# Optimization experiments

Hardware: AMD Instinct MI355X
Metric: run time of the kernel (lower is better)

The kernel has to match this reference:

```python
import jax, jax.numpy as jnp
import numpy as np
import math

B, SES, SEQ, H, K = 16, 16, 64, 512, 32
L = SES * SEQ


def setup_inputs() -> dict:
    key = jax.random.key(0)
    ks = jax.random.split(key, 16)
    s = 1.0 / math.sqrt(H)
    return {
        "user_emb": jax.random.normal(ks[0], (B, H), jnp.float32),
        "item_emb": jax.random.normal(ks[1], (B, SES, SEQ, H), jnp.float32),
        "mask": jnp.zeros((B, L, K), jnp.float32),
        "index": jax.random.randint(ks[2], (L, K), 0, L, jnp.int64),
        "Wq": jax.random.normal(ks[3], (H, H), jnp.float32) * s,
        "bq": jnp.zeros((H,), jnp.float32),
        "Wk": jax.random.normal(ks[4], (H, H), jnp.float32) * s,
        "bk": jnp.zeros((H,), jnp.float32),
        "Wv": jax.random.normal(ks[5], (H, H), jnp.float32) * s,
        "bv": jnp.zeros((H,), jnp.float32),
        "Wd": jax.random.normal(ks[6], (H, H), jnp.float32) * s,
        "bd": jnp.zeros((H,), jnp.float32),
        "ln_g": jnp.ones((H,), jnp.float32),
        "ln_b": jnp.zeros((H,), jnp.float32),
    }


def reference(user_emb, item_emb, mask, index, Wq, bq, Wk, bk, Wv, bv, Wd, bd, ln_g, ln_b):
    b, ses, seq, h = item_emb.shape
    l = ses * seq
    item_flat = item_emb.reshape(b, l, h)
    q = user_emb @ Wq.T + bq                       # [B, H]
    k = item_flat @ Wk.T + bk                      # [B, L, H]
    v = item_flat @ Wv.T + bv                      # [B, L, H]
    # scalar query against all L keys, scaled by sqrt(hidden_size)
    scores = jnp.einsum("bh,blh->bl", q, k) / math.sqrt(h)
    scores = scores[:, index] + mask               # gather -> [B, L, K]
    w = jax.nn.softmax(scores, axis=-1)            # [B, L, K]
    vg = v[:, index, :]                            # gather -> [B, L, K, H]
    attn_out = jnp.einsum("blk,blkh->blh", w, vg)  # [B, L, H]
    dense = attn_out @ Wd.T + bd
    x = dense + item_flat                          # residual (dropout = identity, eval)
    mu = jnp.mean(x, axis=-1, keepdims=True)
    var = jnp.var(x, axis=-1, keepdims=True)
    y = (x - mu) / jnp.sqrt(var + 1e-12) * ln_g + ln_b
    return y.reshape(b, ses, seq, h)
```

## Files before the change

### kernel.cpp

```cpp
#include <hip/hip_runtime.h>
#include <math.h>

constexpr int HD   = 512;
constexpr int LL   = 1024;
constexpr int MT   = 16384;
constexpr int KNBR = 32;
constexpr float SCL = 0.04419417382415922f;

typedef __attribute__((ext_vector_type(8))) short  bf16x8;
typedef __attribute__((ext_vector_type(4))) float  f32x4;

__device__ inline float b2f(unsigned short u) {
    union { unsigned int i; float f; } v; v.i = (unsigned int)u << 16; return v.f;
}
__device__ inline float b2f_lo(unsigned int u) {
    union { unsigned int i; float f; } v; v.i = u << 16; return v.f;
}
__device__ inline float b2f_hi(unsigned int u) {
    union { unsigned int i; float f; } v; v.i = u & 0xffff0000u; return v.f;
}
__device__ inline unsigned short f2b(float x) {
    union { float f; unsigned int u; } v; v.f = x;
    unsigned int r = v.u + 0x7fff + ((v.u >> 16) & 1);
    return (unsigned short)(r >> 16);
}

constexpr int PB_CONV_I = 8192;
constexpr int PB_CONV_W = 512;
constexpr int PB_Q      = 2048;

__global__ __launch_bounds__(256) void prep(
    const float* __restrict__ item, const float* __restrict__ Wv,
    const float* __restrict__ Wd, const float* __restrict__ u,
    const float* __restrict__ Wq, const float* __restrict__ bq,
    unsigned short* __restrict__ item_bf, unsigned short* __restrict__ item_kt,
    unsigned short* __restrict__ Wv_bf, unsigned short* __restrict__ Wd_bf,
    float* __restrict__ q)
{
    const int blk = blockIdx.x, tid = threadIdx.x;

    if (blk < PB_CONV_I) {
        const int i = blk * 1024 + tid * 4;
        float4 v = *(const float4*)&item[i];
        ushort4 o;
        o.x = f2b(v.x); o.y = f2b(v.y); o.z = f2b(v.z); o.w = f2b(v.w);
        *(ushort4*)&item_bf[i] = o;
        const int m = i >> 9, k = i & 511;
        *(ushort4*)&item_kt[((size_t)(k >> 5) * MT + m) * 32 + (k & 31)] = o;
        return;
    }
    if (blk < PB_CONV_I + PB_CONV_W) {
        const int n = HD*HD;
        const int i = (blk - PB_CONV_I) * 1024 + tid * 4;
        const float* s; unsigned short* d; int off;
        if (i < n) { s = Wv; d = Wv_bf; off = i; }
        else       { s = Wd; d = Wd_bf; off = i - n; }
        float4 v = *(const float4*)&s[off];
        ushort4 o;
        o.x = f2b(v.x); o.y = f2b(v.y); o.z = f2b(v.z); o.w = f2b(v.w);
        const int nr = off >> 9, k = off & 511;
        *(ushort4*)&d[((k >> 5) * 512 + nr) * 32 + (k & 31)] = o;
        return;
    }
    {
        const int wid  = (blk - PB_CONV_I - PB_CONV_W) * 4 + (tid >> 6);
        const int lane = tid & 63;
        const int b = wid >> 9, h = wid & 511;
        const float* ur = &u[b*HD + lane*8];
        const float* wr = &Wq[(size_t)h*HD + lane*8];
        const float4 u0 = *(const float4*)ur, u1 = *(const float4*)(ur+4);
        const float4 w0 = *(const float4*)wr, w1 = *(const float4*)(wr+4);
        float acc = u0.x*w0.x + u0.y*w0.y + u0.z*w0.z + u0.w*w0.w
                  + u1.x*w1.x + u1.y*w1.y + u1.z*w1.z + u1.w*w1.w;
        #pragma unroll
        for (int off = 32; off; off >>= 1) acc += __shfl_down(acc, off);
        if (lane == 0) q[b*HD + h] = acc + bq[h];
    }
}

__global__ __launch_bounds__(256) void gemm_v_r(
    const unsigned short* __restrict__ Akt, const unsigned short* __restrict__ Wt,
    const float* __restrict__ bv, const float* __restrict__ Wk,
    const float* __restrict__ bk, const float* __restrict__ q,
    unsigned short* __restrict__ v_bf, float* __restrict__ rbuf,
    float* __restrict__ s0buf)
{
    __shared__ unsigned short As[2][128 * 32];
    __shared__ unsigned short Bs[2][128 * 32];

    const int blk = blockIdx.x;
    const int tid = threadIdx.x;

    if (blk >= 512) {
        if (blk < 640) {
            __shared__ float red[4][64];
            const int rblk = blk - 512;
            const int b = rblk >> 3, c0 = (rblk & 7) * 64;
            const int cl = tid & 63, hg = tid >> 6;
            const float* qb = &q[b*HD];
            const float* wb = &Wk[(size_t)hg*128*HD + c0 + cl];
            float acc = 0.f;
            #pragma unroll 8
            for (int h = 0; h < 128; h++)
                acc += qb[hg*128 + h] * wb[(size_t)h*HD];
            red[hg][cl] = acc;
            __syncthreads();
            if (tid < 64)
                rbuf[b*HD + c0 + tid] = SCL *
                    (red[0][tid] + red[1][tid] + red[2][tid] + red[3][tid]);
        } else {
            __shared__ float sp[4];
            const int b = blk - 640;
            float p = q[b*HD + tid]*bk[tid] + q[b*HD + tid + 256]*bk[tid + 256];
            #pragma unroll
            for (int off = 32; off; off >>= 1) p += __shfl_down(p, off);
            if ((tid & 63) == 0) sp[tid >> 6] = p;
            __syncthreads();
            if (tid == 0) s0buf[b] = (sp[0] + sp[1] + sp[2] + sp[3]) * SCL;
        }
        return;
    }

    const int rowb = (blk & 7) | ((blk >> 5) << 3);
    const int colb = (blk >> 3) & 3;
    const int row0 = rowb * 128;
    const int col0 = colb * 128;

    const int wave = tid >> 6, lane = tid & 63;
    const int wm = (wave >> 1) * 64;
    const int wn = (wave & 1)  * 64;

    const int lrr = lane >> 2;
    const int cc  = lane & 3;
    int st_row[2], st_gchunk[2];
    #pragma unroll
    for (int t = 0; t < 2; t++) {
        const int m = wave*32 + t*16 + lrr;
        st_row[t]    = m;
        st_gchunk[t] = cc ^ ((m >> 1) & 3);
    }

    const int fr   = lane & 15;
    const int quad = lane >> 4;

    f32x4 acc[4][4];
    #pragma unroll
    for (int i = 0; i < 4; i++)
        #pragma unroll
        for (int j = 0; j < 4; j++)
            acc[i][j] = (f32x4){0.f, 0.f, 0.f, 0.f};

    int a_off[4], b_off[4];
    #pragma unroll
    for (int i = 0; i < 4; i++) {
        const int m = wm + i*16 + fr;
        a_off[i] = m*32 + ((quad ^ ((m >> 1) & 3)) << 3);
        const int n = wn + i*16 + fr;
        b_off[i] = n*32 + ((quad ^ ((n >> 1) & 3)) << 3);
    }

    auto stage = [&](int bf, int kt) {
        #pragma unroll
        for (int t = 0; t < 2; t++) {
            const int m = st_row[t];
            const unsigned short* ga =
                &Akt[((size_t)kt*MT + row0 + m)*32 + st_gchunk[t]*8];
            __builtin_amdgcn_global_load_lds(
                (const __attribute__((address_space(1))) void*)ga,
                (__attribute__((address_space(3))) void*)&As[bf][(wave*32 + t*16)*32],
                16, 0, 0);
            const unsigned short* gw =
                &Wt[((size_t)kt*512 + col0 + m)*32 + st_gchunk[t]*8];
            __builtin_amdgcn_global_load_lds(
                (const __attribute__((address_space(1))) void*)gw,
                (__attribute__((address_space(3))) void*)&Bs[bf][(wave*32 + t*16)*32],
                16, 0, 0);
        }
    };

    stage(0, 0);
    stage(1, 1);

    for (int s = 0; s < 15; ++s) {
        asm volatile("s_waitcnt vmcnt(4)" ::: "memory");
        __builtin_amdgcn_s_barrier();
        asm volatile("" ::: "memory");

        const int cur = s & 1;
        bf16x8 af[4], bfr[4];
        #pragma unroll
        for (int i = 0; i < 4; i++) {
            af[i]  = *(const bf16x8*)&As[cur][a_off[i]];
            bfr[i] = *(const bf16x8*)&Bs[cur][b_off[i]];
        }
        asm volatile("s_waitcnt lgkmcnt(0)" ::: "memory");
        __builtin_amdgcn_sched_barrier(0);
        __builtin_amdgcn_s_barrier();

        if (s + 2 < 16) stage(cur, s + 2);

        __builtin_amdgcn_s_setprio(1);
        #pragma unroll
        for (int i = 0; i < 4; i++)
            #pragma unroll
            for (int j = 0; j < 4; j++)
                acc[i][j] = __builtin_amdgcn_mfma_f32_16x16x32_bf16(
                    af[i], bfr[j], acc[i][j], 0, 0, 0);
        __builtin_amdgcn_s_setprio(0);
    }
    {
        asm volatile("s_waitcnt vmcnt(0)" ::: "memory");
        __builtin_amdgcn_s_barrier();
        asm volatile("" ::: "memory");
        bf16x8 af[4], bfr[4];
        #pragma unroll
        for (int i = 0; i < 4; i++) {
            af[i]  = *(const bf16x8*)&As[1][a_off[i]];
            bfr[i] = *(const bf16x8*)&Bs[1][b_off[i]];
        }
        asm volatile("s_waitcnt lgkmcnt(0)" ::: "memory");
        __builtin_amdgcn_sched_barrier(0);
        #pragma unroll
        for (int i = 0; i < 4; i++)
            #pragma unroll
            for (int j = 0; j < 4; j++)
                acc[i][j] = __builtin_amdgcn_mfma_f32_16x16x32_bf16(
                    af[i], bfr[j], acc[i][j], 0, 0, 0);
    }

    #pragma unroll
    for (int j = 0; j < 4; j++) {
        const int col = col0 + wn + j*16 + fr;
        const float bb = bv[col];
        #pragma unroll
        for (int i = 0; i < 4; i++) {
            #pragma unroll
            for (int r = 0; r < 4; r++) {
                const int row = row0 + wm + i*16 + quad*4 + r;
                v_bf[(size_t)row*HD + col] = f2b(acc[i][j][r] + bb);
            }
        }
    }
}

__global__ __launch_bounds__(256) void gp_scores(
    const float* __restrict__ rbuf, const float* __restrict__ s0buf,
    const unsigned short* __restrict__ item_bf, float* __restrict__ scores)
{
    const int m = blockIdx.x * 4 + (threadIdx.x >> 6);
    const int lane = threadIdx.x & 63;
    const int b = m >> 10;
    const unsigned short* ir = &item_bf[(size_t)m*HD + lane*8];
    const uint4 iv = *(const uint4*)ir;
    const float* rr = &rbuf[b*HD + lane*8];
    const float4 r0 = *(const float4*)rr;
    const float4 r1 = *(const float4*)(rr + 4);
    float acc = r0.x*b2f_lo(iv.x) + r0.y*b2f_hi(iv.x)
              + r0.z*b2f_lo(iv.y) + r0.w*b2f_hi(iv.y)
              + r1.x*b2f_lo(iv.z) + r1.y*b2f_hi(iv.z)
              + r1.z*b2f_lo(iv.w) + r1.w*b2f_hi(iv.w);
    #pragma unroll
    for (int off = 32; off; off >>= 1) acc += __shfl_down(acc, off);
    if (lane == 0) scores[m] = acc + s0buf[b];
}

__global__ __launch_bounds__(512, 4) void dense_attn_ln(
    const float* __restrict__ scores, const int* __restrict__ index,
    const float* __restrict__ mask, const unsigned short* __restrict__ v,
    const unsigned short* __restrict__ Wt,
    const float* __restrict__ bd, const unsigned short* __restrict__ res,
    const float* __restrict__ ln_g, const float* __restrict__ ln_b,
    float* __restrict__ out)
{
    __shared__ unsigned short att[32 * 528];
    __shared__ float rsum[8][32], rsq[8][32];

    const int tid  = threadIdx.x;
    const int wave = tid >> 6, lane = tid & 63;
    const int bid  = blockIdx.x;
    const int rblk = (bid & 7) * 64 + (bid >> 3);
    const int row0 = rblk * 32;
    const int b    = row0 >> 10;

    const int fr = lane & 15, quad = lane >> 4;

    const unsigned short* wbase = Wt + ((size_t)wave*64 + fr)*32 + quad*8;
    auto loadW = [&](int kt, bf16x8* dst) {
        #pragma unroll
        for (int j = 0; j < 4; j++)
            dst[j] = *(const bf16x8*)(wbase + (size_t)kt*512*32 + j*16*32);
    };

    bf16x8 wreg[2][4];
    loadW(0, wreg[0]);
    loadW(1, wreg[1]);

    {
        const unsigned short* vb = v + (size_t)b * LL * HD;
        const int loff = lane * 8;
        const int t = lane & 31;
        for (int rr = 0; rr < 4; ++rr) {
            const int lrow = wave * 4 + rr;
            const int m = row0 + lrow;
            const int l = m & 1023;

            const int idx = index[l*KNBR + t];
            const float s = scores[b*LL + idx] + mask[(size_t)m*KNBR + t];

            float mx = s;
            #pragma unroll
            for (int off = 16; off; off >>= 1) mx = fmaxf(mx, __shfl_xor(mx, off));
            const float e = __expf(s - mx);
            float sum = e;
            #pragma unroll
            for (int off = 16; off; off >>= 1) sum += __shfl_xor(sum, off);
            const float w = e / sum;

            float a[8] = {};
            #pragma unroll 8
            for (int t2 = 0; t2 < KNBR; t2++) {
                const int   it = __builtin_amdgcn_readlane(idx, t2);
                const float wt = __int_as_float(
                    __builtin_amdgcn_readlane(__float_as_int(w), t2));
                const uint4 pv = *(const uint4*)(vb + (size_t)it*HD + loff);
                a[0] += wt * b2f_lo(pv.x); a[1] += wt * b2f_hi(pv.x);
                a[2] += wt * b2f_lo(pv.y); a[3] += wt * b2f_hi(pv.y);
                a[4] += wt * b2f_lo(pv.z); a[5] += wt * b2f_hi(pv.z);
                a[6] += wt * b2f_lo(pv.w); a[7] += wt * b2f_hi(pv.w);
            }
            uint4 o;
            o.x = (unsigned int)f2b(a[0]) | ((unsigned int)f2b(a[1]) << 16);
            o.y = (unsigned int)f2b(a[2]) | ((unsigned int)f2b(a[3]) << 16);
            o.z = (unsigned int)f2b(a[4]) | ((unsigned int)f2b(a[5]) << 16);
            o.w = (unsigned int)f2b(a[6]) | ((unsigned int)f2b(a[7]) << 16);
            const int byteoff = lrow*1040 + ((lane*16) ^ ((lrow & 7) << 4));
            *(uint4*)((char*)att + byteoff) = o;
        }
    }
    __syncthreads();

    f32x4 acc[2][4];
    #pragma unroll
    for (int i = 0; i < 2; i++)
        #pragma unroll
        for (int j = 0; j < 4; j++)
            acc[i][j] = (f32x4){0.f, 0.f, 0.f, 0.f};

    int a_row[2];
    #pragma unroll
    for (int i = 0; i < 2; i++) a_row[i] = i*16 + fr;

    #pragma unroll
    for (int s = 0; s < 16; ++s) {
        bf16x8 af[2];
        #pragma unroll
        for (int i = 0; i < 2; i++) {
            const int cb = (s*64 + quad*16) ^ ((a_row[i] & 7) << 4);
            af[i] = *(const bf16x8*)((const char*)att + a_row[i]*1040 + cb);
        }
        bf16x8 cur[4];
        #pragma unroll
        for (int j = 0; j < 4; j++) cur[j] = wreg[s & 1][j];
        #pragma unroll
        for (int i = 0; i < 2; i++)
            #pragma unroll
            for (int j = 0; j < 4; j++)
                acc[i][j] = __builtin_amdgcn_mfma_f32_16x16x32_bf16(
                    af[i], cur[j], acc[i][j], 0, 0, 0);
        if (s + 2 < 16) loadW(s + 2, wreg[s & 1]);
    }
    __syncthreads();

    unsigned short* rs = att;
    #pragma unroll
    for (int u2 = 0; u2 < 4; u2++) {
        const int id = tid*4 + u2;
        const int rr = id >> 6, c8 = id & 63;
        *(uint4*)&rs[rr*528 + c8*8] =
            *(const uint4*)&res[(size_t)(row0 + rr)*HD + c8*8];
    }
    __syncthreads();

    float bdv[4], gv[4], lbv[4];
    #pragma unroll
    for (int j = 0; j < 4; j++) {
        const int col = wave*64 + j*16 + fr;
        bdv[j] = bd[col]; gv[j] = ln_g[col]; lbv[j] = ln_b[col];
    }

    #pragma unroll
    for (int i = 0; i < 2; i++) {
        #pragma unroll
        for (int r = 0; r < 4; r++) {
            const int lrow = i*16 + quad*4 + r;
            float a1 = 0.f, a2 = 0.f;
            #pragma unroll
            for (int j = 0; j < 4; j++) {
                const int col = wave*64 + j*16 + fr;
                float val = acc[i][j][r] + bdv[j] + b2f(rs[lrow*528 + col]);
                acc[i][j][r] = val;
                a1 += val; a2 += val*val;
            }
            #pragma unroll
            for (int off = 1; off < 16; off <<= 1) {
                a1 += __shfl_xor(a1, off);
                a2 += __shfl_xor(a2, off);
            }
            if (fr == 0) { rsum[wave][lrow] = a1; rsq[wave][lrow] = a2; }
        }
    }
    __syncthreads();

    #pragma unroll
    for (int i = 0; i < 2; i++) {
        #pragma unroll
        for (int r = 0; r < 4; r++) {
            const int lrow = i*16 + quad*4 + r;
            float tot = 0.f, tot2 = 0.f;
            #pragma unroll
            for (int w2 = 0; w2 < 8; w2++) {
                tot  += rsum[w2][lrow];
                tot2 += rsq[w2][lrow];
            }
            const float mu  = tot * (1.f/HD);
            const float var = tot2 * (1.f/HD) - mu*mu;
            const float inv = rsqrtf(var + 1e-12f);
            const size_t gr = (size_t)(row0 + lrow) * HD;
            #pragma unroll
            for (int j = 0; j < 4; j++) {
                const int col = wave*64 + j*16 + fr;
                out[gr + col] = (acc[i][j][r] - mu)*inv*gv[j] + lbv[j];
            }
        }
    }
}

extern "C" void kernel_launch(void* const* d_in, const int* in_sizes, int n_in,
                              void* d_out, int out_size, void* d_ws, size_t ws_size,
                              hipStream_t stream) {
    const float* user_emb = (const float*)d_in[0];
    const float* item_emb = (const float*)d_in[1];
    const float* mask     = (const float*)d_in[2];
    const int*   index    = (const int*)  d_in[3];
    const float* Wq = (const float*)d_in[4];  const float* bq = (const float*)d_in[5];
    const float* Wk = (const float*)d_in[6];  const float* bk = (const float*)d_in[7];
    const float* Wv = (const float*)d_in[8];  const float* bv = (const float*)d_in[9];
    const float* Wd = (const float*)d_in[10]; const float* bd = (const float*)d_in[11];
    const float* ln_g = (const float*)d_in[12];
    const float* ln_b = (const float*)d_in[13];

    float* out = (float*)d_out;

    char* p = (char*)d_ws;
    unsigned short* item_bf = (unsigned short*)p; p += (size_t)MT*HD*2;
    unsigned short* item_kt = (unsigned short*)p; p += (size_t)MT*HD*2;
    unsigned short* v_bf    = (unsigned short*)p; p += (size_t)MT*HD*2;
    unsigned short* Wv_bf   = (unsigned short*)p; p += (size_t)HD*HD*2;
    unsigned short* Wd_bf   = (unsigned short*)p; p += (size_t)HD*HD*2;
    float* q      = (float*)p; p += 16*HD*4;
    float* rbuf   = (float*)p; p += 16*HD*4;
    float* s0buf  = (float*)p; p += 16*4;
    float* scores = (float*)p; p += MT*4;

    prep<<<PB_CONV_I + PB_CONV_W + PB_Q, 256, 0, stream>>>(
        item_emb, Wv, Wd, user_emb, Wq, bq,
        item_bf, item_kt, Wv_bf, Wd_bf, q);

    gemm_v_r<<<656, 256, 0, stream>>>(item_kt, Wv_bf, bv, Wk, bk, q,
                                      v_bf, rbuf, s0buf);

    gp_scores<<<MT/4, 256, 0, stream>>>(rbuf, s0buf, item_bf, scores);

    dense_attn_ln<<<512, 512, 0, stream>>>(scores, index, mask, v_bf,
                                           Wd_bf, bd, item_bf,
                                           ln_g, ln_b, out);
}
```

Before: 179.7 us.

## Halve rows per block in dense_attn_ln and batch softmax for two rows

Each block of the fused attention/dense/LayerNorm kernel now handles 16 rows instead of 32, so twice as many blocks launch (1024). Occupancy is raised by a larger launch-bounds minimum, and each wave computes the softmax for its two rows together. The intent is more parallelism across the 256 CUs and better latency hiding for the gathered V loads. The cost is that each block reloads the full Wd weight matrix for half as many rows, doubling total weight traffic, and the MFMA accumulator work per weight load is halved.

```diff
diff --git a/kernel.cpp b/kernel.cpp
--- a/kernel.cpp
+++ b/kernel.cpp
@@ -264,7 +264,7 @@
     if (lane == 0) scores[m] = acc + s0buf[b];
 }
 
-__global__ __launch_bounds__(512, 4) void dense_attn_ln(
+__global__ __launch_bounds__(512, 6) void dense_attn_ln(
     const float* __restrict__ scores, const int* __restrict__ index,
     const float* __restrict__ mask, const unsigned short* __restrict__ v,
     const unsigned short* __restrict__ Wt,
@@ -272,14 +272,14 @@
     const float* __restrict__ ln_g, const float* __restrict__ ln_b,
     float* __restrict__ out)
 {
-    __shared__ unsigned short att[32 * 528];
-    __shared__ float rsum[8][32], rsq[8][32];
+    __shared__ unsigned short att[16 * 528];
+    __shared__ float rsum[8][16], rsq[8][16];
 
     const int tid  = threadIdx.x;
     const int wave = tid >> 6, lane = tid & 63;
     const int bid  = blockIdx.x;
-    const int rblk = (bid & 7) * 64 + (bid >> 3);
-    const int row0 = rblk * 32;
+    const int rblk = (bid & 7) * 128 + (bid >> 3);
+    const int row0 = rblk * 16;
     const int b    = row0 >> 10;
 
     const int fr = lane & 15, quad = lane >> 4;
@@ -299,23 +299,34 @@
         const unsigned short* vb = v + (size_t)b * LL * HD;
         const int loff = lane * 8;
         const int t = lane & 31;
-        for (int rr = 0; rr < 4; ++rr) {
-            const int lrow = wave * 4 + rr;
-            const int m = row0 + lrow;
-            const int l = m & 1023;
-
-            const int idx = index[l*KNBR + t];
-            const float s = scores[b*LL + idx] + mask[(size_t)m*KNBR + t];
-
-            float mx = s;
-            #pragma unroll
-            for (int off = 16; off; off >>= 1) mx = fmaxf(mx, __shfl_xor(mx, off));
-            const float e = __expf(s - mx);
-            float sum = e;
-            #pragma unroll
-            for (int off = 16; off; off >>= 1) sum += __shfl_xor(sum, off);
-            const float w = e / sum;
-
+        const int lrow0 = wave * 2, lrow1 = wave * 2 + 1;
+        const int m0 = row0 + lrow0, m1 = row0 + lrow1;
+
+        const int idx0 = index[(m0 & 1023)*KNBR + t];
+        const int idx1 = index[(m1 & 1023)*KNBR + t];
+        float s0v = scores[b*LL + idx0] + mask[(size_t)m0*KNBR + t];
+        float s1v = scores[b*LL + idx1] + mask[(size_t)m1*KNBR + t];
+
+        float mx0 = s0v, mx1 = s1v;
+        #pragma unroll
+        for (int off = 16; off; off >>= 1) {
+            mx0 = fmaxf(mx0, __shfl_xor(mx0, off));
+            mx1 = fmaxf(mx1, __shfl_xor(mx1, off));
+        }
+        float e0 = __expf(s0v - mx0), e1 = __expf(s1v - mx1);
+        float sm0 = e0, sm1 = e1;
+        #pragma unroll
+        for (int off = 16; off; off >>= 1) {
+            sm0 += __shfl_xor(sm0, off);
+            sm1 += __shfl_xor(sm1, off);
+        }
+        const float w0 = e0 / sm0, w1 = e1 / sm1;
+
+        #pragma unroll
+        for (int rr = 0; rr < 2; ++rr) {
+            const int lrow = wave*2 + rr;
+            const int idx  = rr ? idx1 : idx0;
+            const float w  = rr ? w1 : w0;
             float a[8] = {};
             #pragma unroll 8
             for (int t2 = 0; t2 < KNBR; t2++) {
@@ -339,42 +350,29 @@
     }
     __syncthreads();
 
-    f32x4 acc[2][4];
-    #pragma unroll
-    for (int i = 0; i < 2; i++)
+    f32x4 acc[4];
+    #pragma unroll
+    for (int j = 0; j < 4; j++) acc[j] = (f32x4){0.f, 0.f, 0.f, 0.f};
+
+    #pragma unroll
+    for (int s = 0; s < 16; ++s) {
+        const int cb = (s*64 + quad*16) ^ ((fr & 7) << 4);
+        const bf16x8 af = *(const bf16x8*)((const char*)att + fr*1040 + cb);
+        bf16x8 cur[4];
+        #pragma unroll
+        for (int j = 0; j < 4; j++) cur[j] = wreg[s & 1][j];
         #pragma unroll
         for (int j = 0; j < 4; j++)
-            acc[i][j] = (f32x4){0.f, 0.f, 0.f, 0.f};
-
-    int a_row[2];
-    #pragma unroll
-    for (int i = 0; i < 2; i++) a_row[i] = i*16 + fr;
-
-    #pragma unroll
-    for (int s = 0; s < 16; ++s) {
-        bf16x8 af[2];
-        #pragma unroll
-        for (int i = 0; i < 2; i++) {
-            const int cb = (s*64 + quad*16) ^ ((a_row[i] & 7) << 4);
-            af[i] = *(const bf16x8*)((const char*)att + a_row[i]*1040 + cb);
-        }
-        bf16x8 cur[4];
-        #pragma unroll
-        for (int j = 0; j < 4; j++) cur[j] = wreg[s & 1][j];
-        #pragma unroll
-        for (int i = 0; i < 2; i++)
-            #pragma unroll
-            for (int j = 0; j < 4; j++)
-                acc[i][j] = __builtin_amdgcn_mfma_f32_16x16x32_bf16(
-                    af[i], cur[j], acc[i][j], 0, 0, 0);
+            acc[j] = __builtin_amdgcn_mfma_f32_16x16x32_bf16(
+                af, cur[j], acc[j], 0, 0, 0);
         if (s + 2 < 16) loadW(s + 2, wreg[s & 1]);
     }
     __syncthreads();
 
     unsigned short* rs = att;
     #pragma unroll
-    for (int u2 = 0; u2 < 4; u2++) {
-        const int id = tid*4 + u2;
+    for (int u2 = 0; u2 < 2; u2++) {
+        const int id = tid*2 + u2;
         const int rr = id >> 6, c8 = id & 63;
         *(uint4*)&rs[rr*528 + c8*8] =
             *(const uint4*)&res[(size_t)(row0 + rr)*HD + c8*8];
@@ -389,48 +387,42 @@
     }
 
     #pragma unroll
-    for (int i = 0; i < 2; i++) {
-        #pragma unroll
-        for (int r = 0; r < 4; r++) {
-            const int lrow = i*16 + quad*4 + r;
-            float a1 = 0.f, a2 = 0.f;
-            #pragma unroll
-            for (int j = 0; j < 4; j++) {
-                const int col = wave*64 + j*16 + fr;
-                float val = acc[i][j][r] + bdv[j] + b2f(rs[lrow*528 + col]);
-                acc[i][j][r] = val;
-                a1 += val; a2 += val*val;
-            }
-            #pragma unroll
-            for (int off = 1; off < 16; off <<= 1) {
-                a1 += __shfl_xor(a1, off);
-                a2 += __shfl_xor(a2, off);
-            }
-            if (fr == 0) { rsum[wave][lrow] = a1; rsq[wave][lrow] = a2; }
-        }
+    for (int r = 0; r < 4; r++) {
+        const int lrow = quad*4 + r;
+        float a1 = 0.f, a2 = 0.f;
+        #pragma unroll
+        for (int j = 0; j < 4; j++) {
+            const int col = wave*64 + j*16 + fr;
+            float val = acc[j][r] + bdv[j] + b2f(rs[lrow*528 + col]);
+            acc[j][r] = val;
+            a1 += val; a2 += val*val;
+        }
+        #pragma unroll
+        for (int off = 1; off < 16; off <<= 1) {
+            a1 += __shfl_xor(a1, off);
+            a2 += __shfl_xor(a2, off);
+        }
+        if (fr == 0) { rsum[wave][lrow] = a1; rsq[wave][lrow] = a2; }
     }
     __syncthreads();
 
     #pragma unroll
-    for (int i = 0; i < 2; i++) {
-        #pragma unroll
-        for (int r = 0; r < 4; r++) {
-            const int lrow = i*16 + quad*4 + r;
-            float tot = 0.f, tot2 = 0.f;
-            #pragma unroll
-            for (int w2 = 0; w2 < 8; w2++) {
-                tot  += rsum[w2][lrow];
-                tot2 += rsq[w2][lrow];
-            }
-            const float mu  = tot * (1.f/HD);
-            const float var = tot2 * (1.f/HD) - mu*mu;
-            const float inv = rsqrtf(var + 1e-12f);
-            const size_t gr = (size_t)(row0 + lrow) * HD;
-            #pragma unroll
-            for (int j = 0; j < 4; j++) {
-                const int col = wave*64 + j*16 + fr;
-                out[gr + col] = (acc[i][j][r] - mu)*inv*gv[j] + lbv[j];
-            }
+    for (int r = 0; r < 4; r++) {
+        const int lrow = quad*4 + r;
+        float tot = 0.f, tot2 = 0.f;
+        #pragma unroll
+        for (int w2 = 0; w2 < 8; w2++) {
+            tot  += rsum[w2][lrow];
+            tot2 += rsq[w2][lrow];
+        }
+        const float mu  = tot * (1.f/HD);
+        const float var = tot2 * (1.f/HD) - mu*mu;
+        const float inv = rsqrtf(var + 1e-12f);
+        const size_t gr = (size_t)(row0 + lrow) * HD;
+        #pragma unroll
+        for (int j = 0; j < 4; j++) {
+            const int col = wave*64 + j*16 + fr;
+            out[gr + col] = (acc[j][r] - mu)*inv*gv[j] + lbv[j];
         }
     }
 }
@@ -471,7 +463,7 @@
 
     gp_scores<<<MT/4, 256, 0, stream>>>(rbuf, s0buf, item_bf, scores);
 
-    dense_attn_ln<<<512, 512, 0, stream>>>(scores, index, mask, v_bf,
-                                           Wd_bf, bd, item_bf,
-                                           ln_g, ln_b, out);
-}
+    dense_attn_ln<<<1024, 512, 0, stream>>>(scores, index, mask, v_bf,
+                                            Wd_bf, bd, item_bf,
+                                            ln_g, ln_b, out);
+}
```

Result: slower. 202.0 us (+12.4%).
